# Optimization experiments

Hardware: AMD Instinct MI355X
Metric: run time of the kernel (lower is better)

The kernel has to match this reference:

```python
import jax, jax.numpy as jnp
import numpy as np

D_MODEL, EMB_DIM, ORDER, SEQ_LEN, BATCH = 768, 33, 64, 8192, 2


def setup_inputs() -> dict:
    key = jax.random.key(0)
    ks = jax.random.split(key, 9)
    x = jax.random.normal(ks[0], (BATCH, D_MODEL, SEQ_LEN), dtype=jnp.float32)

    # PositionalEmbedding: t in [0,1], complex exponential bands
    bands = (EMB_DIM - 1) // 2
    t = jnp.linspace(0.0, 1.0, SEQ_LEN, dtype=jnp.float32)[None, :, None]          # (1, L, 1)
    t_rescaled = jnp.linspace(0.0, SEQ_LEN - 1, SEQ_LEN, dtype=jnp.float32)[None, :, None]
    w_ang = 2.0 * jnp.pi * t_rescaled / SEQ_LEN                                     # (1, L, 1)
    f = jnp.linspace(1e-4, bands - 1, bands, dtype=jnp.float32)[None, None]         # (1, 1, bands)
    zc = jnp.exp(-1j * f.astype(jnp.complex64) * w_ang.astype(jnp.complex64))
    z = jnp.concatenate([t, zc.real, zc.imag], axis=-1)                             # (1, L, emb_dim)

    # Sin activation frequency (shared single instance across all MLP layers), w=1
    freq = jnp.ones((1, ORDER), dtype=jnp.float32)

    def lin(k, fan_out, fan_in):
        s = 1.0 / np.sqrt(fan_in)
        return jax.random.normal(k, (fan_out, fan_in), dtype=jnp.float32) * s

    W1 = lin(ks[1], ORDER, EMB_DIM)
    b1 = jax.random.normal(ks[2], (ORDER,), dtype=jnp.float32) * 0.02
    W2 = lin(ks[3], ORDER, ORDER)
    b2 = jax.random.normal(ks[4], (ORDER,), dtype=jnp.float32) * 0.02
    W3 = lin(ks[5], ORDER, ORDER)
    b3 = jax.random.normal(ks[6], (ORDER,), dtype=jnp.float32) * 0.02
    Wout = lin(ks[7], D_MODEL, ORDER)  # no bias

    # ExponentialModulation deltas (deterministic buffer)
    target, fast_pct, slow_pct = 0.01, 0.3, 1.5
    max_decay = np.log(target) / fast_pct
    min_decay = np.log(target) / slow_pct
    deltas = jnp.linspace(min_decay, max_decay, D_MODEL, dtype=jnp.float32)[None, None]  # (1,1,d)

    bias_D = jax.random.normal(ks[8], (D_MODEL,), dtype=jnp.float32)

    return {"x": x, "L": SEQ_LEN, "z": z, "t": t, "freq": freq,
            "W1": W1, "b1": b1, "W2": W2, "b2": b2, "W3": W3, "b3": b3,
            "Wout": Wout, "deltas": deltas, "bias_D": bias_D}


def reference(x, L, z, t, freq, W1, b1, W2, b2, W3, b3, Wout, deltas, bias_D):
    zL, tL = z[:, :L], t[:, :L]                      # (1, L, emb_dim), (1, L, 1)
    # Implicit filter MLP with shared Sin activation
    h = jnp.sin(freq * (jnp.einsum('ble,oe->blo', zL, W1) + b1))
    h = jnp.sin(freq * (jnp.einsum('blo,po->blp', h, W2) + b2))
    h = jnp.sin(freq * (jnp.einsum('blo,po->blp', h, W3) + b3))
    h = jnp.einsum('blo,do->bld', h, Wout)           # (1, L, d_model)
    # Exponential modulation
    h = h * jnp.exp(-tL * jnp.abs(deltas))
    k = h[0].T                                       # (d_model, L)
    # FFT-based long convolution (fftconv_ref with gelu=False).
    # torch: k_f = rfft(k, n)/n ; y = irfft(u_f*k_f, n, norm='forward') == standard irfft(u_f*rfft(k,n), n)
    fft_size = 2 * L
    k_f = jnp.fft.rfft(k, n=fft_size)                # (d_model, n//2+1) complex
    u_f = jnp.fft.rfft(x, n=fft_size)                # (B, d_model, n//2+1)
    y = jnp.fft.irfft(u_f * k_f, n=fft_size)[..., :L]
    out = y + x * bias_D[:, None]
    return out.astype(x.dtype)
```

## Files before the change

kernel.cpp:

```cpp
#include <hip/hip_runtime.h>
#include <hip/hip_fp16.h>
#include <math.h>

#define D_MODEL 768
#define EMB 33
#define ORDER 64
#define SEQ 8192
#define BATCH 2
#define M 8192

#define PI_F 3.14159265358979323846f

#define IDX(a) ((a) + ((a) >> 4) + ((a) >> 7))
#define LDS_SZ 8768

__device__ __forceinline__ int rev13(int x) { return (int)(__brev((unsigned)x) >> 19); }

__device__ __constant__ float C8[8] = {
    1.f, 0.9238795325f, 0.7071067812f, 0.3826834324f,
    0.f, -0.3826834324f, -0.7071067812f, -0.9238795325f };
__device__ __constant__ float S8n[8] = {
    0.f, -0.3826834324f, -0.7071067812f, -0.9238795325f,
    -1.f, -0.9238795325f, -0.7071067812f, -0.3826834324f };
__device__ __constant__ float S8p[8] = {
    0.f, 0.3826834324f, 0.7071067812f, 0.9238795325f,
    1.f, 0.9238795325f, 0.7071067812f, 0.3826834324f };

__global__ __launch_bounds__(256) void mlp_kernel(
    const float* __restrict__ z, const float* __restrict__ freq,
    const float* __restrict__ W1, const float* __restrict__ b1,
    const float* __restrict__ W2, const float* __restrict__ b2,
    const float* __restrict__ W3, const float* __restrict__ b3,
    float* __restrict__ h3T)
{
    __shared__ float zt[33 * 40];
    __shared__ float h1[64 * 42];
    __shared__ float h2[64 * 42];
    __shared__ float Wb[64 * 68];
    __shared__ float sfr[64], sb[64];
    int t = threadIdx.x;
    int l0 = blockIdx.x * 32;

    for (int i = t; i < 32 * 33; i += 256) {
        int l = i / 33, e = i - l * 33;
        zt[e * 40 + l] = z[(size_t)(l0 + l) * 33 + e];
    }
    for (int i = t; i < 64 * 33; i += 256) {
        int o = i / 33, e = i - o * 33;
        Wb[e * 68 + o] = W1[i];
    }
    if (t < 64) { sfr[t] = freq[t]; sb[t] = b1[t]; }
    __syncthreads();

    int lx = t & 15, oy = t >> 4;
    float fr4[4], bi4[4], acc[2][4];
#pragma unroll
    for (int i = 0; i < 4; ++i) { fr4[i] = sfr[4 * oy + i]; bi4[i] = sb[4 * oy + i]; }
#pragma unroll
    for (int c = 0; c < 2; ++c)
#pragma unroll
        for (int i = 0; i < 4; ++i) acc[c][i] = bi4[i];
    for (int e = 0; e < 33; ++e) {
        float2 hv = *(const float2*)&zt[e * 40 + 2 * lx];
        float4 wv = *(const float4*)&Wb[e * 68 + 4 * oy];
        float h[2] = {hv.x, hv.y}, w[4] = {wv.x, wv.y, wv.z, wv.w};
#pragma unroll
        for (int c = 0; c < 2; ++c)
#pragma unroll
            for (int i = 0; i < 4; ++i) acc[c][i] = fmaf(h[c], w[i], acc[c][i]);
    }
#pragma unroll
    for (int i = 0; i < 4; ++i) {
        float2 v = make_float2(__sinf(fr4[i] * acc[0][i]), __sinf(fr4[i] * acc[1][i]));
        *(float2*)&h1[(4 * oy + i) * 42 + 2 * lx] = v;
    }
    __syncthreads();

    for (int i = t; i < 4096; i += 256) {
        int o = i >> 6, q = i & 63;
        Wb[q * 68 + o] = W2[i];
    }
    if (t < 64) sb[t] = b2[t];
    __syncthreads();
#pragma unroll
    for (int i = 0; i < 4; ++i) bi4[i] = sb[4 * oy + i];
#pragma unroll
    for (int c = 0; c < 2; ++c)
#pragma unroll
        for (int i = 0; i < 4; ++i) acc[c][i] = bi4[i];
    for (int q = 0; q < 64; ++q) {
        float2 hv = *(const float2*)&h1[q * 42 + 2 * lx];
        float4 wv = *(const float4*)&Wb[q * 68 + 4 * oy];
        float h[2] = {hv.x, hv.y}, w[4] = {wv.x, wv.y, wv.z, wv.w};
#pragma unroll
        for (int c = 0; c < 2; ++c)
#pragma unroll
            for (int i = 0; i < 4; ++i) acc[c][i] = fmaf(h[c], w[i], acc[c][i]);
    }
#pragma unroll
    for (int i = 0; i < 4; ++i) {
        float2 v = make_float2(__sinf(fr4[i] * acc[0][i]), __sinf(fr4[i] * acc[1][i]));
        *(float2*)&h2[(4 * oy + i) * 42 + 2 * lx] = v;
    }
    __syncthreads();

    for (int i = t; i < 4096; i += 256) {
        int o = i >> 6, q = i & 63;
        Wb[q * 68 + o] = W3[i];
    }
    if (t < 64) sb[t] = b3[t];
    __syncthreads();
#pragma unroll
    for (int i = 0; i < 4; ++i) bi4[i] = sb[4 * oy + i];
#pragma unroll
    for (int c = 0; c < 2; ++c)
#pragma unroll
        for (int i = 0; i < 4; ++i) acc[c][i] = bi4[i];
    for (int q = 0; q < 64; ++q) {
        float2 hv = *(const float2*)&h2[q * 42 + 2 * lx];
        float4 wv = *(const float4*)&Wb[q * 68 + 4 * oy];
        float h[2] = {hv.x, hv.y}, w[4] = {wv.x, wv.y, wv.z, wv.w};
#pragma unroll
        for (int c = 0; c < 2; ++c)
#pragma unroll
            for (int i = 0; i < 4; ++i) acc[c][i] = fmaf(h[c], w[i], acc[c][i]);
    }
#pragma unroll
    for (int i = 0; i < 4; ++i) {
        float2 v = make_float2(__sinf(fr4[i] * acc[0][i]), __sinf(fr4[i] * acc[1][i]));
        *(float2*)&h3T[(size_t)(4 * oy + i) * SEQ + l0 + 2 * lx] = v;
    }
}

__global__ __launch_bounds__(256) void filt_kernel(
    const float* __restrict__ h3T, const float* __restrict__ Wout,
    const float* __restrict__ tvec, const float* __restrict__ deltas,
    float* __restrict__ kout)
{
    __shared__ float ht[64 * 132];
    __shared__ float wt[64 * 68];
    int t = threadIdx.x;
    int l0 = blockIdx.x * 128, d0 = blockIdx.y * 64;

    for (int i = t; i < 64 * 128; i += 256) {
        int o = i >> 7, l = i & 127;
        ht[o * 132 + l] = h3T[(size_t)o * SEQ + l0 + l];
    }
    for (int i = t; i < 4096; i += 256) {
        int dd = i >> 6, kk = i & 63;
        wt[kk * 68 + dd] = Wout[(size_t)(d0 + dd) * 64 + kk];
    }
    __syncthreads();

    int lx = t & 31, dy = t >> 5;
    float acc[4][8];
#pragma unroll
    for (int c = 0; c < 4; ++c)
#pragma unroll
        for (int i = 0; i < 8; ++i) acc[c][i] = 0.f;
    for (int kk = 0; kk < 64; ++kk) {
        float4 hv = *(const float4*)&ht[kk * 132 + 4 * lx];
        float4 w0 = *(const float4*)&wt[kk * 68 + 8 * dy];
        float4 w1 = *(const float4*)&wt[kk * 68 + 8 * dy + 4];
        float h[4] = {hv.x, hv.y, hv.z, hv.w};
        float w[8] = {w0.x, w0.y, w0.z, w0.w, w1.x, w1.y, w1.z, w1.w};
#pragma unroll
        for (int c = 0; c < 4; ++c)
#pragma unroll
            for (int i = 0; i < 8; ++i) acc[c][i] = fmaf(h[c], w[i], acc[c][i]);
    }

    float4 tl4 = *(const float4*)&tvec[l0 + 4 * lx];
    float tl[4] = {tl4.x, tl4.y, tl4.z, tl4.w};
    float del[8];
#pragma unroll
    for (int i = 0; i < 8; ++i) del[i] = fabsf(deltas[d0 + 8 * dy + i]);
#pragma unroll
    for (int i = 0; i < 8; ++i) {
        int d = d0 + 8 * dy + i;
        float4 v = make_float4(acc[0][i] * __expf(-tl[0] * del[i]),
                               acc[1][i] * __expf(-tl[1] * del[i]),
                               acc[2][i] * __expf(-tl[2] * del[i]),
                               acc[3][i] * __expf(-tl[3] * del[i]));
        *(float4*)&kout[(size_t)d * SEQ + l0 + 4 * lx] = v;
    }
}

template<int H>
__device__ __forceinline__ void fwd8g1(float2* A, int i, float c1, float s1)
{
    constexpr int H4 = H / 4;
    float c2 = c1 * c1 - s1 * s1, s2 = 2.f * c1 * s1;
    float c3 = c2 * c2 - s2 * s2, s3 = 2.f * c2 * s2;
    float xr[8], xi[8];
    int ad[8];
#pragma unroll
    for (int m = 0; m < 8; ++m) {
        ad[m] = IDX(i + m * H4);
        float2 v = A[ad[m]];
        xr[m] = v.x; xi[m] = v.y;
    }
    const float r = 0.70710678118f;
    float twc[4], tws[4];
    twc[0] = c1;            tws[0] = s1;
    twc[1] = r * (c1 + s1); tws[1] = r * (s1 - c1);
    twc[2] = s1;            tws[2] = -c1;
    twc[3] = r * (s1 - c1); tws[3] = -r * (c1 + s1);
#pragma unroll
    for (int m = 0; m < 4; ++m) {
        float ur = xr[m] + xr[m + 4], ui = xi[m] + xi[m + 4];
        float dr = xr[m] - xr[m + 4], di = xi[m] - xi[m + 4];
        xr[m] = ur; xi[m] = ui;
        xr[m + 4] = dr * twc[m] - di * tws[m];
        xi[m + 4] = dr * tws[m] + di * twc[m];
    }
#pragma unroll
    for (int base = 0; base < 8; base += 4)
#pragma unroll
        for (int mm = 0; mm < 2; ++mm) {
            int a = base + mm, b = a + 2;
            float ur = xr[a] + xr[b], ui = xi[a] + xi[b];
            float dr = xr[a] - xr[b], di = xi[a] - xi[b];
            xr[a] = ur; xi[a] = ui;
            if (mm == 0) { xr[b] = dr * c2 - di * s2; xi[b] = dr * s2 + di * c2; }
            else         { xr[b] = dr * s2 + di * c2; xi[b] = di * s2 - dr * c2; }
        }
#pragma unroll
    for (int m = 0; m < 8; m += 2) {
        float ur = xr[m] + xr[m + 1], ui = xi[m] + xi[m + 1];
        float dr = xr[m] - xr[m + 1], di = xi[m] - xi[m + 1];
        xr[m] = ur; xi[m] = ui;
        xr[m + 1] = dr * c3 - di * s3; xi[m + 1] = dr * s3 + di * c3;
    }
#pragma unroll
    for (int m = 0; m < 8; ++m) A[ad[m]] = make_float2(xr[m], xi[m]);
}

template<int H>
__device__ __forceinline__ void inv8g1(float2* A, int i, float c, float s)
{
    float c2 = c * c - s * s, s2 = 2.f * c * s;
    float c4 = c2 * c2 - s2 * s2, s4 = 2.f * c2 * s2;
    float xr[8], xi[8]; int ad[8];
#pragma unroll
    for (int m = 0; m < 8; ++m) {
        ad[m] = IDX(i + m * H);
        float2 v = A[ad[m]];
        xr[m] = v.x; xi[m] = v.y;
    }
#pragma unroll
    for (int m = 0; m < 8; m += 2) {
        float tr = xr[m + 1] * c4 - xi[m + 1] * s4;
        float ti = xr[m + 1] * s4 + xi[m + 1] * c4;
        xr[m + 1] = xr[m] - tr; xi[m + 1] = xi[m] - ti;
        xr[m]     = xr[m] + tr; xi[m]     = xi[m] + ti;
    }
#pragma unroll
    for (int base = 0; base < 8; base += 4)
#pragma unroll
        for (int mm = 0; mm < 2; ++mm) {
            int a = base + mm, b = a + 2;
            float tr, ti;
            if (mm == 0) { tr = xr[b] * c2 - xi[b] * s2; ti = xr[b] * s2 + xi[b] * c2; }
            else         { tr = -(xr[b] * s2 + xi[b] * c2); ti = xr[b] * c2 - xi[b] * s2; }
            xr[b] = xr[a] - tr; xi[b] = xi[a] - ti;
            xr[a] = xr[a] + tr; xi[a] = xi[a] + ti;
        }
    const float r = 0.70710678118f;
    float t3c[4], t3s[4];
    t3c[0] = c;            t3s[0] = s;
    t3c[1] = r * (c - s);  t3s[1] = r * (c + s);
    t3c[2] = -s;           t3s[2] = c;
    t3c[3] = -r * (c + s); t3s[3] = r * (c - s);
#pragma unroll
    for (int m = 0; m < 4; ++m) {
        float tr = xr[m + 4] * t3c[m] - xi[m + 4] * t3s[m];
        float ti = xr[m + 4] * t3s[m] + xi[m + 4] * t3c[m];
        xr[m + 4] = xr[m] - tr; xi[m + 4] = xi[m] - ti;
        xr[m]     = xr[m] + tr; xi[m]     = xi[m] + ti;
    }
#pragma unroll
    for (int m = 0; m < 8; ++m) A[ad[m]] = make_float2(xr[m], xi[m]);
}

__device__ __forceinline__ void fft_fwd(float2* A, int t)
{
    {
        float c1, s1;
        __sincosf((-PI_F / 4096.0f) * (float)t, &s1, &c1);
        fwd8g1<4096>(A, t, c1, s1);
        const float cR = 0.9238795325f, sR = -0.3826834324f;
        fwd8g1<4096>(A, t + 512, c1 * cR - s1 * sR, s1 * cR + c1 * sR);
    }
    __syncthreads();
    {
        int w = t >> 6, l = t & 63, base = w << 10;
        float ca, sa;
        __sincosf((-PI_F / 512.0f) * (float)l, &sa, &ca);
        fwd8g1<512>(A, base + l, ca, sa);
        const float cR = 0.9238795325f, sR = -0.3826834324f;
        fwd8g1<512>(A, base + 64 + l, ca * cR - sa * sR, sa * cR + ca * sR);

        float cb, sb;
        __sincosf((-PI_F / 64.0f) * (float)(l & 15), &sb, &cb);
        int i0 = base + ((l & ~15) << 3) + (l & 15);
        fwd8g1<64>(A, i0, cb, sb);
        fwd8g1<64>(A, i0 + 512, cb, sb);

        int pb = IDX(16 * t);
        float fr[16], fi[16];
#pragma unroll
        for (int e = 0; e < 16; ++e) { float2 v = A[pb + e]; fr[e] = v.x; fi[e] = v.y; }
#pragma unroll
        for (int k = 0; k < 8; ++k) {
            float cs = C8[k], sn = S8n[k];
            float arr = fr[k], aii = fi[k], brr = fr[k + 8], bii = fi[k + 8];
            fr[k] = arr + brr; fi[k] = aii + bii;
            float dr = arr - brr, di = aii - bii;
            fr[k + 8] = dr * cs - di * sn; fi[k + 8] = dr * sn + di * cs;
        }
#pragma unroll
        for (int b0 = 0; b0 < 16; b0 += 8)
#pragma unroll
            for (int k = 0; k < 4; ++k) {
                float cs = C8[2 * k], sn = S8n[2 * k];
                int i1 = b0 + k, i2 = i1 + 4;
                float arr = fr[i1], aii = fi[i1], brr = fr[i2], bii = fi[i2];
                fr[i1] = arr + brr; fi[i1] = aii + bii;
                float dr = arr - brr, di = aii - bii;
                fr[i2] = dr * cs - di * sn; fi[i2] = dr * sn + di * cs;
            }
#pragma unroll
        for (int b0 = 0; b0 < 16; b0 += 4)
#pragma unroll
            for (int k = 0; k < 2; ++k) {
                float cs = C8[4 * k], sn = S8n[4 * k];
                int i1 = b0 + k, i2 = i1 + 2;
                float arr = fr[i1], aii = fi[i1], brr = fr[i2], bii = fi[i2];
                fr[i1] = arr + brr; fi[i1] = aii + bii;
                float dr = arr - brr, di = aii - bii;
                fr[i2] = dr * cs - di * sn; fi[i2] = dr * sn + di * cs;
            }
#pragma unroll
        for (int b0 = 0; b0 < 16; b0 += 2) {
            float arr = fr[b0], aii = fi[b0], brr = fr[b0 + 1], bii = fi[b0 + 1];
            fr[b0] = arr + brr; fi[b0] = aii + bii;
            fr[b0 + 1] = arr - brr; fi[b0 + 1] = aii - bii;
        }
#pragma unroll
        for (int e = 0; e < 16; ++e) A[pb + e] = make_float2(fr[e], fi[e]);
    }
    __syncthreads();
}

__device__ __forceinline__ void fft_inv(float2* A, int t)
{
    {
        int pb = IDX(16 * t);
        float fr[16], fi[16];
#pragma unroll
        for (int e = 0; e < 16; ++e) { float2 v = A[pb + e]; fr[e] = v.x; fi[e] = v.y; }
#pragma unroll
        for (int b0 = 0; b0 < 16; b0 += 2) {
            float arr = fr[b0], aii = fi[b0], brr = fr[b0 + 1], bii = fi[b0 + 1];
            fr[b0] = arr + brr; fi[b0] = aii + bii;
            fr[b0 + 1] = arr - brr; fi[b0 + 1] = aii - bii;
        }
#pragma unroll
        for (int b0 = 0; b0 < 16; b0 += 4)
#pragma unroll
            for (int k = 0; k < 2; ++k) {
                float cs = C8[4 * k], sn = S8p[4 * k];
                int i1 = b0 + k, i2 = i1 + 2;
                float arr = fr[i1], aii = fi[i1], brr = fr[i2], bii = fi[i2];
                float tr = brr * cs - bii * sn, ti = brr * sn + bii * cs;
                fr[i1] = arr + tr; fi[i1] = aii + ti;
                fr[i2] = arr - tr; fi[i2] = aii - ti;
            }
#pragma unroll
        for (int b0 = 0; b0 < 16; b0 += 8)
#pragma unroll
            for (int k = 0; k < 4; ++k) {
                float cs = C8[2 * k], sn = S8p[2 * k];
                int i1 = b0 + k, i2 = i1 + 4;
                float arr = fr[i1], aii = fi[i1], brr = fr[i2], bii = fi[i2];
                float tr = brr * cs - bii * sn, ti = brr * sn + bii * cs;
                fr[i1] = arr + tr; fi[i1] = aii + ti;
                fr[i2] = arr - tr; fi[i2] = aii - ti;
            }
#pragma unroll
        for (int k = 0; k < 8; ++k) {
            float cs = C8[k], sn = S8p[k];
            float arr = fr[k], aii = fi[k], brr = fr[k + 8], bii = fi[k + 8];
            float tr = brr * cs - bii * sn, ti = brr * sn + bii * cs;
            fr[k] = arr + tr; fi[k] = aii + ti;
            fr[k + 8] = arr - tr; fi[k + 8] = aii - ti;
        }
#pragma unroll
        for (int e = 0; e < 16; ++e) A[pb + e] = make_float2(fr[e], fi[e]);

        int w = t >> 6, l = t & 63, base = w << 10;
        float ca, sa;
        __sincosf((PI_F / 64.0f) * (float)(l & 15), &sa, &ca);
        int i0 = base + ((l & ~15) << 3) + (l & 15);
        inv8g1<16>(A, i0, ca, sa);
        inv8g1<16>(A, i0 + 512, ca, sa);

        float cb, sb;
        __sincosf((PI_F / 512.0f) * (float)l, &sb, &cb);
        inv8g1<128>(A, base + l, cb, sb);
        const float cR = 0.9238795325f, sR = 0.3826834324f;
        inv8g1<128>(A, base + 64 + l, cb * cR - sb * sR, sb * cR + cb * sR);
    }
    __syncthreads();
    {
        float c1, s1;
        __sincosf((PI_F / 4096.0f) * (float)t, &s1, &c1);
        inv8g1<1024>(A, t, c1, s1);
        const float cR = 0.9238795325f, sR = 0.3826834324f;
        inv8g1<1024>(A, t + 512, c1 * cR - s1 * sR, s1 * cR + c1 * sR);
    }
    __syncthreads();
}

__global__ __launch_bounds__(512, 4) void kf_kernel(
    float* outk, float* kb0, float* kb1)
{
    __shared__ float2 A[LDS_SZ];
    int t = threadIdx.x, d = blockIdx.x;
    const float* kp = outk + (size_t)d * SEQ;
    for (int n = t; n < 4096; n += 512) {
        A[IDX(n)] = ((const float2*)kp)[n];
    }
    for (int n = 4096 + t; n < M; n += 512) A[IDX(n)] = make_float2(0.f, 0.f);
    __syncthreads();
    fft_fwd(A, t);

    __half2* P0 = (__half2*)(kb0 + (size_t)d * SEQ);
    __half2* P1 = (__half2*)(kb1 + (size_t)d * SEQ);
    bool dup = (kb1 != kb0);
    float cs, sn;
    __sincosf(-PI_F * (float)t * (1.0f / 8192.0f), &sn, &cs);
    const float cRo = 0.9807852804f, sRo = -0.1950903220f;
    for (int j = t; j <= 4096; j += 512) {
        int jm = (M - j) & (M - 1);
        int p0 = rev13(j), p1 = rev13(jm);
        float2 z1 = A[IDX(p0)], z2 = A[IDX(p1)];
        float Ar_ = 0.5f * (z1.x + z2.x), Ai_ = 0.5f * (z1.y - z2.y);
        float Br_ = 0.5f * (z1.y + z2.y), Bi_ = 0.5f * (z2.x - z1.x);
        float wbr = cs * Br_ - sn * Bi_, wbi = cs * Bi_ + sn * Br_;
        float K1r = Ar_ + wbr, K1i = Ai_ + wbi;
        float K2r = Ar_ - wbr, K2i = -(Ai_ - wbi);
        if (j == 0) {
            __half2 v = __floats2half2_rn(K1r, K2r);
            P0[0] = v; if (dup) P1[0] = v;
        } else {
            __half2 v1 = __floats2half2_rn(K1r, K1i);
            P0[j] = v1; if (dup) P1[j] = v1;
            if (j != 4096) {
                __half2 v2 = __floats2half2_rn(K2r, K2i);
                P0[M - j] = v2; if (dup) P1[M - j] = v2;
            }
        }
        float cn = cs * cRo - sn * sRo; sn = sn * cRo + cs * sRo; cs = cn;
    }
}

__global__ __launch_bounds__(512, 4) void conv_kernel(
    const float* __restrict__ x, const float* __restrict__ bias,
    float* outk, const float* __restrict__ kbase, int kstride)
{
    __shared__ float2 A[LDS_SZ];
    int t = threadIdx.x, d = blockIdx.x, b = blockIdx.y;
    const float* xp = x + ((size_t)(b * D_MODEL + d)) * SEQ;
    float bd = bias[d];

#pragma unroll
    for (int idx = 0; idx < 8; ++idx) {
        int n = t + (idx << 9);
        A[IDX(n)] = ((const float2*)xp)[n];
    }
    for (int n = 4096 + t; n < M; n += 512) A[IDX(n)] = make_float2(0.f, 0.f);
    __syncthreads();
    fft_fwd(A, t);

    const __half2* P = (const __half2*)(kbase + (size_t)(b * kstride + d) * SEQ);
    float cs, sn;
    __sincosf(-PI_F * (float)t * (1.0f / 8192.0f), &sn, &cs);
    const float cRo = 0.9807852804f, sRo = -0.1950903220f;
    for (int j = t; j <= 4096; j += 512) {
        int jm = (M - j) & (M - 1);
        int p0 = rev13(j), p1 = rev13(jm);
        int q0 = IDX(p0), q1 = IDX(p1);
        float2 z1 = A[q0], z2 = A[q1];
        float Ar_ = 0.5f * (z1.x + z2.x), Ai_ = 0.5f * (z1.y - z2.y);
        float Br_ = 0.5f * (z1.y + z2.y), Bi_ = 0.5f * (z2.x - z1.x);
        float wbr = cs * Br_ - sn * Bi_, wbi = cs * Bi_ + sn * Br_;
        float U1r = Ar_ + wbr, U1i = Ai_ + wbi;
        float U2r = Ar_ - wbr, U2i = -(Ai_ - wbi);
        float K1r, K1i, K2r, K2i;
        if (j == 0) {
            __half2 v = P[0];
            K1r = __low2float(v) + bd;  K1i = 0.f;
            K2r = __high2float(v) + bd; K2i = 0.f;
        } else {
            __half2 v1 = P[j];
            __half2 v2 = P[M - j];
            K1r = __low2float(v1) + bd; K1i = __high2float(v1);
            K2r = __low2float(v2) + bd; K2i = __high2float(v2);
        }
        float P1r = U1r * K1r - U1i * K1i, P1i = U1r * K1i + U1i * K1r;
        float P2r = U2r * K2r - U2i * K2i, P2i = U2r * K2i + U2i * K2r;
        float Er = 0.5f * (P1r + P2r), Ei = 0.5f * (P1i - P2i);
        float Or = 0.5f * (P1r - P2r), Oi = 0.5f * (P1i + P2i);
        float G = cs * Oi - sn * Or;
        float H = cs * Or + sn * Oi;
        A[q0] = make_float2(Er - G, Ei + H);
        if (j != 0) A[q1] = make_float2(Er + G, -Ei + H);
        float cn = cs * cRo - sn * sRo; sn = sn * cRo + cs * sRo; cs = cn;
    }
    __syncthreads();
    fft_inv(A, t);

    const float invM = 1.0f / 8192.0f;
    float* op = outk + ((size_t)(b * D_MODEL + d)) * SEQ;
#pragma unroll
    for (int idx = 0; idx < 8; ++idx) {
        int n = t + (idx << 9);
        float2 v = A[IDX(n)];
        float2 ov;
        ov.x = v.x * invM;
        ov.y = v.y * invM;
        ((float2*)op)[n] = ov;
    }
}

extern "C" void kernel_launch(void* const* d_in, const int* in_sizes, int n_in,
                              void* d_out, int out_size, void* d_ws, size_t ws_size,
                              hipStream_t stream)
{
    (void)in_sizes; (void)n_in; (void)out_size;
    const float* x      = (const float*)d_in[0];
    const float* z      = (const float*)d_in[2];
    const float* tvec   = (const float*)d_in[3];
    const float* freq   = (const float*)d_in[4];
    const float* W1     = (const float*)d_in[5];
    const float* b1     = (const float*)d_in[6];
    const float* W2     = (const float*)d_in[7];
    const float* b2     = (const float*)d_in[8];
    const float* W3     = (const float*)d_in[9];
    const float* b3     = (const float*)d_in[10];
    const float* Wout   = (const float*)d_in[11];
    const float* deltas = (const float*)d_in[12];
    const float* bias   = (const float*)d_in[13];
    float* out = (float*)d_out;

    float* h3T = out + ((size_t)(2 * D_MODEL - 64) * SEQ);
    float* k   = out;

    const size_t kbytes = (size_t)D_MODEL * SEQ * sizeof(float);
    bool usews = (d_ws != nullptr) && (ws_size >= kbytes);
    float* kws = (float*)d_ws;
    float* kb0 = usews ? kws : out;
    float* kb1 = usews ? kws : out + (size_t)D_MODEL * SEQ;
    const float* kbase = usews ? kws : out;
    int kstride = usews ? 0 : D_MODEL;

    hipLaunchKernelGGL(mlp_kernel, dim3(SEQ / 32), dim3(256), 0, stream,
                       z, freq, W1, b1, W2, b2, W3, b3, h3T);
    hipLaunchKernelGGL(filt_kernel, dim3(SEQ / 128, D_MODEL / 64), dim3(256), 0, stream,
                       h3T, Wout, tvec, deltas, k);
    hipLaunchKernelGGL(kf_kernel, dim3(D_MODEL), dim3(512), 0, stream,
                       out, kb0, kb1);
    hipLaunchKernelGGL(conv_kernel, dim3(D_MODEL, BATCH), dim3(512), 0, stream,
                       x, bias, out, kbase, kstride);
}
```

Measured before the change: 226.9 us.

## Fuse implicit-filter MLP and Wout projection into one kernel

Merges the MLP kernel and the filter projection/modulation kernel, so the third MLP layer output stays in shared memory instead of going through a global scratch buffer. Each 32-position block then loops over all 12 d_model tiles, reloading Wout tiles into shared memory and writing the modulated filter directly. This removes one launch and the h3T global round trip. In exchange, only 256 blocks do the projection work, with smaller per-thread tiles and extra syncs, so parallelism and reuse of Wout loads across blocks drop.

```diff
diff --git a/kernel.cpp b/kernel.cpp
--- a/kernel.cpp
+++ b/kernel.cpp
@@ -26,12 +26,13 @@
     0.f, 0.3826834324f, 0.7071067812f, 0.9238795325f,
     1.f, 0.9238795325f, 0.7071067812f, 0.3826834324f };
 
-__global__ __launch_bounds__(256) void mlp_kernel(
+__global__ __launch_bounds__(256) void mlpfilt_kernel(
     const float* __restrict__ z, const float* __restrict__ freq,
     const float* __restrict__ W1, const float* __restrict__ b1,
     const float* __restrict__ W2, const float* __restrict__ b2,
     const float* __restrict__ W3, const float* __restrict__ b3,
-    float* __restrict__ h3T)
+    const float* __restrict__ Wout, const float* __restrict__ tvec,
+    const float* __restrict__ deltas, float* __restrict__ kout)
 {
     __shared__ float zt[33 * 40];
     __shared__ float h1[64 * 42];
@@ -128,61 +129,42 @@
 #pragma unroll
     for (int i = 0; i < 4; ++i) {
         float2 v = make_float2(__sinf(fr4[i] * acc[0][i]), __sinf(fr4[i] * acc[1][i]));
-        *(float2*)&h3T[(size_t)(4 * oy + i) * SEQ + l0 + 2 * lx] = v;
-    }
-}
-
-__global__ __launch_bounds__(256) void filt_kernel(
-    const float* __restrict__ h3T, const float* __restrict__ Wout,
-    const float* __restrict__ tvec, const float* __restrict__ deltas,
-    float* __restrict__ kout)
-{
-    __shared__ float ht[64 * 132];
-    __shared__ float wt[64 * 68];
-    int t = threadIdx.x;
-    int l0 = blockIdx.x * 128, d0 = blockIdx.y * 64;
-
-    for (int i = t; i < 64 * 128; i += 256) {
-        int o = i >> 7, l = i & 127;
-        ht[o * 132 + l] = h3T[(size_t)o * SEQ + l0 + l];
-    }
-    for (int i = t; i < 4096; i += 256) {
-        int dd = i >> 6, kk = i & 63;
-        wt[kk * 68 + dd] = Wout[(size_t)(d0 + dd) * 64 + kk];
-    }
-    __syncthreads();
-
-    int lx = t & 31, dy = t >> 5;
-    float acc[4][8];
-#pragma unroll
-    for (int c = 0; c < 4; ++c)
-#pragma unroll
-        for (int i = 0; i < 8; ++i) acc[c][i] = 0.f;
-    for (int kk = 0; kk < 64; ++kk) {
-        float4 hv = *(const float4*)&ht[kk * 132 + 4 * lx];
-        float4 w0 = *(const float4*)&wt[kk * 68 + 8 * dy];
-        float4 w1 = *(const float4*)&wt[kk * 68 + 8 * dy + 4];
-        float h[4] = {hv.x, hv.y, hv.z, hv.w};
-        float w[8] = {w0.x, w0.y, w0.z, w0.w, w1.x, w1.y, w1.z, w1.w};
-#pragma unroll
-        for (int c = 0; c < 4; ++c)
-#pragma unroll
-            for (int i = 0; i < 8; ++i) acc[c][i] = fmaf(h[c], w[i], acc[c][i]);
-    }
-
-    float4 tl4 = *(const float4*)&tvec[l0 + 4 * lx];
-    float tl[4] = {tl4.x, tl4.y, tl4.z, tl4.w};
-    float del[8];
-#pragma unroll
-    for (int i = 0; i < 8; ++i) del[i] = fabsf(deltas[d0 + 8 * dy + i]);
-#pragma unroll
-    for (int i = 0; i < 8; ++i) {
-        int d = d0 + 8 * dy + i;
-        float4 v = make_float4(acc[0][i] * __expf(-tl[0] * del[i]),
-                               acc[1][i] * __expf(-tl[1] * del[i]),
-                               acc[2][i] * __expf(-tl[2] * del[i]),
-                               acc[3][i] * __expf(-tl[3] * del[i]));
-        *(float4*)&kout[(size_t)d * SEQ + l0 + 4 * lx] = v;
+        *(float2*)&h1[(4 * oy + i) * 42 + 2 * lx] = v;
+    }
+    __syncthreads();
+
+    float2 tl2 = *(const float2*)&tvec[l0 + 2 * lx];
+    for (int dt = 0; dt < 12; ++dt) {
+        int d0 = dt * 64;
+        for (int i = t; i < 4096; i += 256) {
+            int dd = i >> 6, kk = i & 63;
+            Wb[kk * 68 + dd] = Wout[(size_t)(d0 + dd) * 64 + kk];
+        }
+        __syncthreads();
+
+        float fa[2][4];
+#pragma unroll
+        for (int c = 0; c < 2; ++c)
+#pragma unroll
+            for (int i = 0; i < 4; ++i) fa[c][i] = 0.f;
+        for (int kk = 0; kk < 64; ++kk) {
+            float2 hv = *(const float2*)&h1[kk * 42 + 2 * lx];
+            float4 wv = *(const float4*)&Wb[kk * 68 + 4 * oy];
+            float h[2] = {hv.x, hv.y}, w[4] = {wv.x, wv.y, wv.z, wv.w};
+#pragma unroll
+            for (int c = 0; c < 2; ++c)
+#pragma unroll
+                for (int i = 0; i < 4; ++i) fa[c][i] = fmaf(h[c], w[i], fa[c][i]);
+        }
+#pragma unroll
+        for (int i = 0; i < 4; ++i) {
+            int d = d0 + 4 * oy + i;
+            float del = fabsf(deltas[d]);
+            float2 v = make_float2(fa[0][i] * __expf(-tl2.x * del),
+                                   fa[1][i] * __expf(-tl2.y * del));
+            *(float2*)&kout[(size_t)d * SEQ + l0 + 2 * lx] = v;
+        }
+        __syncthreads();
     }
 }
 
@@ -555,8 +537,7 @@
     const float* bias   = (const float*)d_in[13];
     float* out = (float*)d_out;
 
-    float* h3T = out + ((size_t)(2 * D_MODEL - 64) * SEQ);
-    float* k   = out;
+    float* k = out;
 
     const size_t kbytes = (size_t)D_MODEL * SEQ * sizeof(float);
     bool usews = (d_ws != nullptr) && (ws_size >= kbytes);
@@ -566,10 +547,8 @@
     const float* kbase = usews ? kws : out;
     int kstride = usews ? 0 : D_MODEL;
 
-    hipLaunchKernelGGL(mlp_kernel, dim3(SEQ / 32), dim3(256), 0, stream,
-                       z, freq, W1, b1, W2, b2, W3, b3, h3T);
-    hipLaunchKernelGGL(filt_kernel, dim3(SEQ / 128, D_MODEL / 64), dim3(256), 0, stream,
-                       h3T, Wout, tvec, deltas, k);
+    hipLaunchKernelGGL(mlpfilt_kernel, dim3(SEQ / 32), dim3(256), 0, stream,
+                       z, freq, W1, b1, W2, b2, W3, b3, Wout, tvec, deltas, k);
     hipLaunchKernelGGL(kf_kernel, dim3(D_MODEL), dim3(512), 0, stream,
                        out, kb0, kb1);
     hipLaunchKernelGGL(conv_kernel, dim3(D_MODEL, BATCH), dim3(512), 0, stream,
```

New measurement: 240.8 us. 1.06x slower.
